# Performance work log

Measured on AMD Instinct MI355X. Metric: run time of the kernel, lower is better.

The kernel has to match this reference:

```python
import jax, jax.numpy as jnp
import numpy as np

B, S, NH = 8, 32, 8
N = S * S + 1            # 1 extra (cls) token + S*S image tokens
C = 512
D = C // NH
SCALE = D ** -0.5
LAM = 0.6


def _ln(x, w, b, eps=1e-5):
    m = x.mean(-1, keepdims=True)
    v = ((x - m) ** 2).mean(-1, keepdims=True)
    return (x - m) / jnp.sqrt(v + eps) * w + b


def _rel_index():
    ch, cw = np.meshgrid(np.arange(S), np.arange(S), indexing='ij')
    cf = np.stack([ch.ravel(), cw.ravel()])            # [2, S*S]
    rel = (cf[:, :, None] - cf[:, None, :]).transpose(1, 2, 0).astype(np.int64)
    rel[..., 0] += S - 1
    rel[..., 1] += S - 1
    rel[..., 0] *= 2 * S - 1
    idx = rel.sum(-1)                                  # [n, n]
    out = np.zeros((N, N), dtype=np.int64)             # F.pad with 0 for extra token row/col
    out[1:, 1:] = idx
    return jnp.asarray(out)


def setup_inputs():
    key = jax.random.key(0)
    ks = jax.random.split(key, 8)
    std = 0.02
    return {
        'x': jax.random.normal(ks[0], (B, N, C), jnp.float32),
        'ln1_w': jnp.ones((C,), jnp.float32), 'ln1_b': jnp.zeros((C,), jnp.float32),
        'qkv_w': jax.random.normal(ks[1], (3 * C, C), jnp.float32) * std,
        'rpb_table': jax.random.normal(ks[2], ((2 * S - 1) * (2 * S - 1) + 1, NH), jnp.float32) * std,
        'proj_w': jax.random.normal(ks[3], (C, C), jnp.float32) * std,
        'proj_b': jnp.zeros((C,), jnp.float32),
        'token_weights': jnp.array([0.5, 0.5], jnp.float32),
        'ln2_w': jnp.ones((C,), jnp.float32), 'ln2_b': jnp.zeros((C,), jnp.float32),
        'fc1_w': jax.random.normal(ks[4], (4 * C, C), jnp.float32) * std,
        'fc1_b': jnp.zeros((4 * C,), jnp.float32),
        'fc2_w': jax.random.normal(ks[5], (C, 4 * C), jnp.float32) * std,
        'fc2_b': jnp.zeros((C,), jnp.float32),
        'rel_index': _rel_index(),
        'H': S, 'W': S,
    }


def _attn_core(xn, qkv_w, rpb_table, rel_index):
    qkv = (xn @ qkv_w.T).reshape(B, N, 3, NH, D).transpose(2, 0, 3, 1, 4)
    q, k, v = qkv[0] * SCALE, qkv[1], qkv[2]           # [B, NH, N, D]
    bias = rpb_table[rel_index].transpose(2, 0, 1)     # [NH, N, N] bias-table gather
    attn = jax.nn.softmax(jnp.einsum('bhnd,bhmd->bhnm', q, k) + bias[None], axis=-1)
    out = jnp.einsum('bhnm,bhmd->bhnd', attn, v).transpose(0, 2, 1, 3).reshape(B, N, C)
    return attn, out


def _plan(attn, token_weights):
    # Non-differentiable token-selection plan (pure index computation).
    a = np.asarray(attn)
    cls = a[:, :, 0, 1:].mean(axis=1)                  # [B, n] head-averaged cls->image attn
    n = cls.shape[1]
    avg = cls.mean(1, keepdims=True)
    mx = cls.max(1, keepdims=True)
    counts = ((cls >= avg) & (cls <= mx)).sum(1)
    max_value = int(counts.max())
    T = float(counts.mean())
    sig = 1.0 / (1.0 + np.exp(-(max_value - T) / B))
    keep = int(round(n * (LAM + (1.0 - LAM) * sig)))
    top = np.argsort(-cls, axis=1)[:, :keep].reshape(-1)   # per-batch top-k, flattened
    _, first = np.unique(top, return_index=True)
    sel = top[np.sort(first)][:keep]                   # dedup (first occurrence), truncate
    remaining = N - (1 + keep)
    w = np.asarray(jax.nn.softmax(token_weights))
    nt = int(w[0] * remaining)
    ni = remaining - nt
    kk = jax.random.key(1234)
    ti = jax.random.randint(kk, (B, nt), 0, 1)         # text pool has exactly 1 token
    ii = jax.random.randint(jax.random.fold_in(kk, 1), (B, ni), 0, n - 1)
    return jnp.asarray(sel), ti, ii


def _gather_tok(t, idx):
    return jnp.take_along_axis(t, jnp.broadcast_to(idx[:, :, None], idx.shape + (t.shape[-1],)), axis=1)


def _assemble(xo, xn, sel, ti, ii):
    parts = [xo[:, :1], xo[:, 1:][:, sel],             # kept extra + selected image tokens
             _gather_tok(xn[:, 1:2], ti),              # random 'text' filler from y=xn
             _gather_tok(xn[:, 2:], ii)]               # random 'image' filler from y=xn
    return jnp.concatenate(parts, axis=1)


def reference(x, ln1_w, ln1_b, qkv_w, rpb_table, proj_w, proj_b, token_weights, ln2_w, ln2_b, fc1_w, fc1_b, fc2_w, fc2_b, rel_index, H, W):
    xn = _ln(x, ln1_w, ln1_b)
    attn, out = _attn_core(xn, qkv_w, rpb_table, rel_index)
    xo = out @ proj_w.T + proj_b
    sel, ti, ii = _plan(attn, token_weights)
    x1 = x + _assemble(xo, xn, sel, ti, ii)
    h = _ln(x1, ln2_w, ln2_b)
    h = jax.nn.gelu(h @ fc1_w.T + fc1_b, approximate=False)
    return x1 + (h @ fc2_w.T + fc2_b)
```

## Files before the change

### kernel.cpp

```cpp
#include <hip/hip_runtime.h>
#include <cmath>

#define PARTITIONABLE 1

constexpr int B_ = 8;
constexpr int N_ = 1025;
constexpr int C_ = 512;
constexpr int NH_ = 8;
constexpr int D_ = 64;
constexpr int K3_ = 1536;
constexpr int F_ = 2048;
constexpr int ROWS_ = B_ * N_;
constexpr int NXCD_ = 8;
constexpr int WCONV_BLKS_ = (K3_ * C_ + C_ * C_ + F_ * C_ + C_ * F_) / 1024;

constexpr size_t BYTE_XN      = 0;
constexpr size_t BYTE_QKVBF   = 16793600;
constexpr size_t BYTE_XNBF    = 41984000;
constexpr size_t BYTE_HBUF    = 16793600;
constexpr size_t BYTE_WTAIL   = 60882944;
constexpr size_t BYTE_ATTNBF  = 67174400;
constexpr size_t BYTE_X1NBF   = 75571200;
constexpr size_t BYTE_XO      = 83968000;
constexpr size_t BYTE_X1      = 100761600;
constexpr size_t PLAN_BYTE    = 117555200;

typedef unsigned short u16;
typedef __attribute__((ext_vector_type(4))) unsigned short u16x4;
typedef __attribute__((ext_vector_type(8))) short bf16x8;
typedef __attribute__((ext_vector_type(4))) float f32x4;

__device__ inline u16 f2bf(float f) {
  unsigned u = __float_as_uint(f);
  u = (u + 0x7FFFu + ((u >> 16) & 1u)) >> 16;
  return (u16)u;
}
__device__ inline float bf2f(u16 u) { return __uint_as_float(((unsigned)u) << 16); }

__device__ inline int xcd_swz(int bid, int nwg) {
  const int xcd = bid % NXCD_, i = bid / NXCD_;
  const int q = nwg / NXCD_, r = nwg % NXCD_;
  const int base = (xcd < r) ? xcd * (q + 1) : r * (q + 1) + (xcd - r) * q;
  return base + i;
}

__device__ inline void gload_lds16(const void* g, void* l) {
  __builtin_amdgcn_global_load_lds(
      (const __attribute__((address_space(1))) void*)g,
      (__attribute__((address_space(3))) void*)l, 16, 0, 0);
}

__global__ __launch_bounds__(256) void ln_wconv_kernel(
    const float* __restrict__ x, const float* __restrict__ w,
    const float* __restrict__ b, float* __restrict__ of, u16* __restrict__ ob,
    const float* __restrict__ w0, const float* __restrict__ w1,
    const float* __restrict__ w2, const float* __restrict__ w3,
    u16* __restrict__ o0, u16* __restrict__ o1,
    u16* __restrict__ o2, u16* __restrict__ o3) {
  __shared__ float red[4];
  if (blockIdx.x >= ROWS_) {
    constexpr int n0 = K3_ * C_, n1 = C_ * C_, n2 = F_ * C_;
    const int idx4 = ((blockIdx.x - ROWS_) * 256 + threadIdx.x) * 4;
    const float* src;
    u16* dst;
    int off;
    if (idx4 < n0) { src = w0; dst = o0; off = idx4; }
    else if (idx4 < n0 + n1) { src = w1; dst = o1; off = idx4 - n0; }
    else if (idx4 < n0 + n1 + n2) { src = w2; dst = o2; off = idx4 - n0 - n1; }
    else { src = w3; dst = o3; off = idx4 - n0 - n1 - n2; }
    const float4 v = *(const float4*)(src + off);
    u16x4 r;
    r.x = f2bf(v.x); r.y = f2bf(v.y); r.z = f2bf(v.z); r.w = f2bf(v.w);
    *(u16x4*)(dst + off) = r;
    return;
  }
  const int r = blockIdx.x;
  const int t = threadIdx.x;
  const float* xr = x + (size_t)r * C_;
  float v0 = xr[t], v1 = xr[t + 256];
  float s = v0 + v1;
#pragma unroll
  for (int o = 32; o; o >>= 1) s += __shfl_down(s, o);
  if ((t & 63) == 0) red[t >> 6] = s;
  __syncthreads();
  const float mean = (red[0] + red[1] + red[2] + red[3]) * (1.0f / 512.0f);
  __syncthreads();
  const float d0 = v0 - mean, d1 = v1 - mean;
  float q = d0 * d0 + d1 * d1;
#pragma unroll
  for (int o = 32; o; o >>= 1) q += __shfl_down(q, o);
  if ((t & 63) == 0) red[t >> 6] = q;
  __syncthreads();
  const float var = (red[0] + red[1] + red[2] + red[3]) * (1.0f / 512.0f);
  const float inv = 1.0f / sqrtf(var + 1e-5f);
  const float r0 = d0 * inv * w[t] + b[t];
  const float r1 = d1 * inv * w[t + 256] + b[t + 256];
  of[(size_t)r * C_ + t] = r0;
  of[(size_t)r * C_ + t + 256] = r1;
  ob[(size_t)r * C_ + t] = f2bf(r0);
  ob[(size_t)r * C_ + t + 256] = f2bf(r1);
}

template <int BN, int ACT, bool RES, bool OUTBF, bool QSCALE, bool PLANQ0>
__global__ __launch_bounds__(256) void gemm_bf_kernel(
    const u16* __restrict__ A, const u16* __restrict__ W,
    const float* __restrict__ bias, const float* __restrict__ resid,
    void* __restrict__ outp, int M, int K, int Nout, int ngemm,
    const float* __restrict__ xnf, const float* __restrict__ qkvwf,
    double* __restrict__ q0o) {
  constexpr int WN = BN / 2;
  constexpr int NJ = WN / 16;
  constexpr int BPW = (BN / 8) / 4;
  __shared__ alignas(16) u16 As[2][128][64];
  __shared__ alignas(16) u16 Bs[2][BN][64];
  if (PLANQ0 && (int)blockIdx.x >= ngemm) {
    const int idx = ((int)blockIdx.x - ngemm) * 256 + threadIdx.x;
    const int b = idx >> 9, hd = idx & 511;
    const float* xr = xnf + (size_t)(b * N_) * C_;
    const float* wr = qkvwf + (size_t)hd * C_;
    double s = 0.0;
    for (int c = 0; c < C_; c += 4) {
      const float4 xv = *(const float4*)(xr + c);
      const float4 wv = *(const float4*)(wr + c);
      s += (double)xv.x * (double)wv.x;
      s += (double)xv.y * (double)wv.y;
      s += (double)xv.z * (double)wv.z;
      s += (double)xv.w * (double)wv.w;
    }
    q0o[idx] = s * 0.125;
    return;
  }
  const int tid = threadIdx.x;
  const int ny = Nout / BN;
  const int l = xcd_swz(blockIdx.x, ngemm);
  const int m0 = (l / ny) * 128, n0 = (l % ny) * BN;
  const int wave = tid >> 6, lane = tid & 63;
  const int wr = wave >> 1, wc = wave & 1;
  const int lrow = lane & 15, lgrp = lane >> 4;
  const int srow = lane >> 3;
  const int soff = (16 * (lane & 7)) ^ (16 * srow);
  const int nk = K >> 6;

  auto stage = [&](int k0, int bufi) {
#pragma unroll
    for (int c = 0; c < 4; ++c) {
      const int q = wave * 4 + c;
      const int row = q * 8 + srow;
      int gm = m0 + row;
      if (gm >= M) gm = M - 1;
      gload_lds16((const char*)(A + (size_t)gm * K + k0) + soff,
                  (char*)&As[bufi][0][0] + (q << 10));
    }
#pragma unroll
    for (int c = 0; c < BPW; ++c) {
      const int q = wave * BPW + c;
      const int row = q * 8 + srow;
      gload_lds16((const char*)(W + (size_t)(n0 + row) * K + k0) + soff,
                  (char*)&Bs[bufi][0][0] + (q << 10));
    }
  };

  f32x4 acc[4][NJ] = {};
  stage(0, 0);
  int buf = 0;
  for (int t = 0; t < nk; ++t) {
    if (t + 1 < nk) {
      stage((t + 1) << 6, buf ^ 1);
      if constexpr (BN == 128) asm volatile("s_waitcnt vmcnt(8)" ::: "memory");
      else                     asm volatile("s_waitcnt vmcnt(6)" ::: "memory");
    } else {
      asm volatile("s_waitcnt vmcnt(0)" ::: "memory");
    }
    __builtin_amdgcn_sched_barrier(0);
    __builtin_amdgcn_s_barrier();
    const char* asb = (const char*)&As[buf][0][0];
    const char* bsb = (const char*)&Bs[buf][0][0];
    __builtin_amdgcn_s_setprio(1);
#pragma unroll
    for (int ch = 0; ch < 2; ++ch) {
      bf16x8 af[4], bfv[NJ];
#pragma unroll
      for (int i = 0; i < 4; ++i) {
        const int ra = wr * 64 + i * 16 + lrow;
        const int cb = ch * 64 + lgrp * 16;
        af[i] = *(const bf16x8*)(asb + (ra << 7) + (cb ^ ((ra & 7) << 4)));
      }
#pragma unroll
      for (int j = 0; j < NJ; ++j) {
        const int rb = wc * WN + j * 16 + lrow;
        const int cb = ch * 64 + lgrp * 16;
        bfv[j] = *(const bf16x8*)(bsb + (rb << 7) + (cb ^ ((rb & 7) << 4)));
      }
#pragma unroll
      for (int i = 0; i < 4; ++i)
#pragma unroll
        for (int j = 0; j < NJ; ++j)
          acc[i][j] = __builtin_amdgcn_mfma_f32_16x16x32_bf16(af[i], bfv[j], acc[i][j], 0, 0, 0);
    }
    __builtin_amdgcn_s_setprio(0);
    asm volatile("s_waitcnt lgkmcnt(0)" ::: "memory");
    __builtin_amdgcn_sched_barrier(0);
    __builtin_amdgcn_s_barrier();
    buf ^= 1;
  }
#pragma unroll
  for (int i = 0; i < 4; ++i) {
#pragma unroll
    for (int j = 0; j < NJ; ++j) {
#pragma unroll
      for (int reg = 0; reg < 4; ++reg) {
        const int gm = m0 + wr * 64 + i * 16 + lgrp * 4 + reg;
        if (gm >= M) continue;
        const int gn = n0 + wc * WN + j * 16 + lrow;
        float v = acc[i][j][reg];
        if (bias) v += bias[gn];
        if (ACT == 1) v = 0.5f * v * (1.0f + erff(v * 0.70710678118654752440f));
        if (QSCALE) { if (gn < 512) v *= 0.125f; }
        if (RES) v += resid[(size_t)gm * Nout + gn];
        if (OUTBF) ((u16*)outp)[(size_t)gm * Nout + gn] = f2bf(v);
        else       ((float*)outp)[(size_t)gm * Nout + gn] = v;
      }
    }
  }
}

__global__ __launch_bounds__(256) void pack_kv_kernel(const u16* __restrict__ qkvbf,
                                                      u16* __restrict__ kb,
                                                      u16* __restrict__ vb,
                                                      const float* __restrict__ qkvwf,
                                                      const double* __restrict__ q0,
                                                      double* __restrict__ u,
                                                      int npack) {
  if ((int)blockIdx.x >= npack) {
    const int idx = ((int)blockIdx.x - npack) * 256 + threadIdx.x;
    const int b = idx >> 12, h = (idx >> 9) & 7, c = idx & 511;
    double s = 0.0;
    for (int d = 0; d < D_; ++d)
      s += q0[b * 512 + h * 64 + d] * (double)qkvwf[(size_t)(512 + h * 64 + d) * C_ + c];
    u[idx] = s;
    return;
  }
  const int tile = blockIdx.x & 15, h = (blockIdx.x >> 4) & 7, b = (int)blockIdx.x >> 7;
  const int t = threadIdx.x;
  __shared__ u16 Vt[64][72];
  const int krow = tile * 64 + (t >> 2);
  const int dseg = (t & 3) * 16;
  const u16* p = qkvbf + (size_t)(b * N_ + krow) * K3_ + 512 + h * D_ + dseg;
  const bf16x8 k0 = *(const bf16x8*)p;
  const bf16x8 k1 = *(const bf16x8*)(p + 8);
  u16* kp = kb + ((size_t)(b * NH_ + h) * 1024 + krow) * 64 + dseg;
  *(bf16x8*)kp = k0;
  *(bf16x8*)(kp + 8) = k1;
  const bf16x8 v0 = *(const bf16x8*)(p + 512);
  const bf16x8 v1 = *(const bf16x8*)(p + 520);
  *(bf16x8*)(&Vt[t >> 2][dseg]) = v0;
  *(bf16x8*)(&Vt[t >> 2][dseg + 8]) = v1;
  __syncthreads();
  const int d = t >> 2, kseg = (t & 3) * 16;
  bf16x8 o0, o1;
#pragma unroll
  for (int i = 0; i < 8; ++i) o0[i] = (short)Vt[kseg + i][d];
#pragma unroll
  for (int i = 0; i < 8; ++i) o1[i] = (short)Vt[kseg + 8 + i][d];
  u16* vp = vb + ((size_t)(b * NH_ + h) * 64 + d) * 1024 + tile * 64 + kseg;
  *(bf16x8*)vp = o0;
  *(bf16x8*)(vp + 8) = o1;
}

__global__ __launch_bounds__(384) void attn_mfma_kernel(
    const u16* __restrict__ qkvbf, const u16* __restrict__ kb,
    const u16* __restrict__ vb, const float* __restrict__ rpb,
    u16* __restrict__ attnout) {
  const int l = xcd_swz(blockIdx.x, gridDim.x);
  const int qt = l % 11;
  const int bh = l / 11;
  const int h = bh & 7, b = bh >> 3;
  const int wave = threadIdx.x >> 6, lane = threadIdx.x & 63;
  const int lrow = lane & 15, lgrp = lane >> 4;
  const int qblk = qt * 96;
  const int qbase = qblk + wave * 16;
  __shared__ alignas(16) u16 Ks[2][64][64];
  __shared__ alignas(16) u16 Vs[2][64][64];
  __shared__ alignas(16) u16 Pl[6][16][74];
  __shared__ u16 tab[36 * 63];

  const u16* kpan = kb + (size_t)(b * NH_ + h) * 1024 * 64;
  const u16* vpan = vb + (size_t)(b * NH_ + h) * 64 * 1024;

  if (wave < 4) {
#pragma unroll
    for (int c = 0; c < 2; ++c) {
      const int q = wave * 2 + c;
      const int Y = (q << 10) | (lane << 4);
      const int Ys = Y ^ (((Y >> 7) & 7) << 4);
      gload_lds16((const char*)kpan + Ys, (char*)&Ks[0][0][0] + (q << 10));
    }
  } else {
#pragma unroll
    for (int c = 0; c < 4; ++c) {
      const int q = (wave - 4) * 4 + c;
      const int Y = (q << 10) | (lane << 4);
      const int Ys = Y ^ (((Y >> 7) & 7) << 4);
      const int row = Y >> 7;
      gload_lds16((const char*)vpan + (size_t)row * 2048 + (Ys & 127),
                  (char*)&Vs[0][0][0] + (q << 10));
    }
  }

  const int qimin = max(qblk - 1, 0);
  const int qimax = min(qblk + 94, 1023);
  const int qymin = qimin >> 5;
  const int qymax = qimax >> 5;
  const int nrows = qymax - qymin + 32;
  for (int i = threadIdx.x; i < nrows * 63; i += 384)
    tab[i] = f2bf(rpb[(size_t)(qymin * 63 + i) * NH_ + h]);

  u16 (*pl)[74] = Pl[wave];

  bf16x8 qf[2];
  {
    const int qrow = min(qbase + lrow, N_ - 1);
    const u16* qp = qkvbf + (size_t)(b * N_ + qrow) * K3_ + h * D_;
    qf[0] = *(const bf16x8*)(qp + lgrp * 8);
    qf[1] = *(const bf16x8*)(qp + 32 + lgrp * 8);
  }

  const float bias0 = rpb[h];

  int AlocR[4];
  bool qclsR[4];
#pragma unroll
  for (int reg = 0; reg < 4; ++reg) {
    const int qr = min(qbase + lgrp * 4 + reg, N_ - 1);
    const int qi = max(qr - 1, 0);
    AlocR[reg] = ((qi >> 5) - qymin + 31) * 63 + (qi & 31) + 31;
    qclsR[reg] = (qr == 0);
  }

  f32x4 psum = {0.f, 0.f, 0.f, 0.f};
  f32x4 o[4] = {};

  __syncthreads();

  for (int t = 0; t < 16; ++t) {
    const int buf = t & 1;
    if (t < 15) {
      const int keybase2 = (t + 1) * 64;
      if (wave < 4) {
#pragma unroll
        for (int c = 0; c < 2; ++c) {
          const int q = wave * 2 + c;
          const int Y = (q << 10) | (lane << 4);
          const int Ys = Y ^ (((Y >> 7) & 7) << 4);
          gload_lds16((const char*)kpan + ((size_t)keybase2 << 7) + Ys,
                      (char*)&Ks[buf ^ 1][0][0] + (q << 10));
        }
        asm volatile("s_waitcnt vmcnt(2)" ::: "memory");
      } else {
#pragma unroll
        for (int c = 0; c < 4; ++c) {
          const int q = (wave - 4) * 4 + c;
          const int Y = (q << 10) | (lane << 4);
          const int Ys = Y ^ (((Y >> 7) & 7) << 4);
          const int row = Y >> 7;
          gload_lds16((const char*)vpan + (size_t)row * 2048 + ((size_t)keybase2 << 1) + (Ys & 127),
                      (char*)&Vs[buf ^ 1][0][0] + (q << 10));
        }
        asm volatile("s_waitcnt vmcnt(4)" ::: "memory");
      }
    } else {
      asm volatile("s_waitcnt vmcnt(0)" ::: "memory");
    }
    __builtin_amdgcn_sched_barrier(0);
    __builtin_amdgcn_s_barrier();

    const int keybase = t * 64;
    const char* ksb = (const char*)&Ks[buf][0][0];
    const char* vsb = (const char*)&Vs[buf][0][0];

    f32x4 s[4] = {};
    __builtin_amdgcn_s_setprio(1);
#pragma unroll
    for (int tile = 0; tile < 4; ++tile) {
      const int row = tile * 16 + lrow;
      const int sw = (row & 7) << 4;
      const bf16x8 kf0 = *(const bf16x8*)(ksb + ((row * 128 + lgrp * 16) ^ sw));
      const bf16x8 kf1 = *(const bf16x8*)(ksb + ((row * 128 + 64 + lgrp * 16) ^ sw));
      s[tile] = __builtin_amdgcn_mfma_f32_16x16x32_bf16(qf[0], kf0, s[tile], 0, 0, 0);
      s[tile] = __builtin_amdgcn_mfma_f32_16x16x32_bf16(qf[1], kf1, s[tile], 0, 0, 0);
    }
    __builtin_amdgcn_s_setprio(0);
#pragma unroll
    for (int tile = 0; tile < 4; ++tile) {
      const int key = keybase + tile * 16 + lrow;
      const int ki = max(key - 1, 0);
      const int kpart = (ki >> 5) * 63 + (ki & 31);
      const bool kcls = (key == 0);
#pragma unroll
      for (int reg = 0; reg < 4; ++reg) {
        const float bias = (qclsR[reg] || kcls) ? bias0 : bf2f(tab[AlocR[reg] - kpart]);
        const float p = __expf(s[tile][reg] + bias);
        psum[reg] += p;
        pl[lgrp * 4 + reg][tile * 16 + lrow] = f2bf(p);
      }
    }
    __builtin_amdgcn_s_setprio(1);
#pragma unroll
    for (int ch = 0; ch < 2; ++ch) {
      const bf16x8 pf = *(const bf16x8*)(&pl[lrow][ch * 32 + lgrp * 8]);
#pragma unroll
      for (int dt = 0; dt < 4; ++dt) {
        const int row = dt * 16 + lrow;
        const bf16x8 vf = *(const bf16x8*)(vsb + ((row * 128 + ch * 64 + lgrp * 16) ^ ((row & 7) << 4)));
        o[dt] = __builtin_amdgcn_mfma_f32_16x16x32_bf16(pf, vf, o[dt], 0, 0, 0);
      }
    }
    __builtin_amdgcn_s_setprio(0);
    asm volatile("s_waitcnt lgkmcnt(0)" ::: "memory");
    __builtin_amdgcn_sched_barrier(0);
    __builtin_amdgcn_s_barrier();
  }

#pragma unroll
  for (int reg = 0; reg < 4; ++reg) {
    float v = psum[reg];
    v += __shfl_xor(v, 1);
    v += __shfl_xor(v, 2);
    v += __shfl_xor(v, 4);
    v += __shfl_xor(v, 8);
    psum[reg] = v;
  }

  float ptail;
  {
    const u16* k1p = qkvbf + (size_t)(b * N_ + 1024) * K3_ + 512 + h * D_;
    const bf16x8 k10 = *(const bf16x8*)(k1p + lgrp * 8);
    const bf16x8 k11 = *(const bf16x8*)(k1p + 32 + lgrp * 8);
    float part = 0.f;
#pragma unroll
    for (int i = 0; i < 8; ++i)
      part += bf2f((u16)qf[0][i]) * bf2f((u16)k10[i]) + bf2f((u16)qf[1][i]) * bf2f((u16)k11[i]);
    part += __shfl_xor(part, 16);
    part += __shfl_xor(part, 32);
    const int q_s = min(qbase + lrow, N_ - 1);
    const int qi_s = max(q_s - 1, 0);
    const int Aloc_s = ((qi_s >> 5) - qymin + 31) * 63 + (qi_s & 31) + 31;
    const float btail = (q_s == 0) ? bias0 : bf2f(tab[Aloc_s - 31 * 63 - 31]);
    ptail = __expf(part + btail);
  }

  float v1024[4];
#pragma unroll
  for (int dt = 0; dt < 4; ++dt)
    v1024[dt] = bf2f(qkvbf[(size_t)(b * N_ + 1024) * K3_ + 1024 + h * D_ + dt * 16 + lrow]);

#pragma unroll
  for (int reg = 0; reg < 4; ++reg) {
    const float pr = __shfl(ptail, lgrp * 4 + reg);
    const int qrow = qbase + lgrp * 4 + reg;
    if (qrow >= N_) continue;
    const float inv = 1.0f / (psum[reg] + pr);
    u16* op = attnout + (size_t)(b * N_ + qrow) * C_ + h * D_ + lrow;
#pragma unroll
    for (int dt = 0; dt < 4; ++dt)
      op[dt * 16] = f2bf((o[dt][reg] + pr * v1024[dt]) * inv);
  }
}

__global__ __launch_bounds__(128) void plan_logit_kernel(const float* __restrict__ xn,
                                                         const double* __restrict__ u,
                                                         double* __restrict__ lgt) {
  __shared__ double ul[8][512];
  const int b = blockIdx.y;
  const int m = blockIdx.x * 128 + threadIdx.x;
  for (int i = threadIdx.x; i < 4096; i += 128)
    ((double*)ul)[i] = u[(size_t)b * 4096 + i];
  __syncthreads();
  if (m >= N_) return;
  const float* xr = xn + (size_t)(b * N_ + m) * C_;
  double s[8] = {};
  for (int c = 0; c < C_; c += 4) {
    const float4 xv = *(const float4*)(xr + c);
#pragma unroll
    for (int hh = 0; hh < 8; ++hh) {
      s[hh] += (double)xv.x * ul[hh][c];
      s[hh] += (double)xv.y * ul[hh][c + 1];
      s[hh] += (double)xv.z * ul[hh][c + 2];
      s[hh] += (double)xv.w * ul[hh][c + 3];
    }
  }
#pragma unroll
  for (int hh = 0; hh < 8; ++hh)
    lgt[(size_t)(b * 8 + hh) * N_ + m] = s[hh];
}

__global__ __launch_bounds__(256) void plan_softmax_kernel(const double* __restrict__ lgt,
                                                           double* __restrict__ mxz) {
  __shared__ double red[4];
  const int bh = blockIdx.x, t = threadIdx.x;
  const double* row = lgt + (size_t)bh * N_;
  double m = -1e300;
  for (int i = t; i < N_; i += 256) m = fmax(m, row[i]);
#pragma unroll
  for (int o = 32; o; o >>= 1) m = fmax(m, __shfl_down(m, o));
  if ((t & 63) == 0) red[t >> 6] = m;
  __syncthreads();
  const double mx = fmax(fmax(red[0], red[1]), fmax(red[2], red[3]));
  __syncthreads();
  double z = 0.0;
  for (int i = t; i < N_; i += 256) z += exp(row[i] - mx);
#pragma unroll
  for (int o = 32; o; o >>= 1) z += __shfl_down(z, o);
  if ((t & 63) == 0) red[t >> 6] = z;
  __syncthreads();
  if (t == 0) {
    mxz[bh] = mx;
    mxz[64 + bh] = red[0] + red[1] + red[2] + red[3];
  }
}

__global__ __launch_bounds__(256) void plan_cls_kernel(const double* __restrict__ lgt,
                                                       const double* __restrict__ mxz,
                                                       double* __restrict__ cls) {
  const int idx = blockIdx.x * 256 + threadIdx.x;
  const int b = idx >> 10, i = idx & 1023;
  double s = 0.0;
  for (int h = 0; h < 8; ++h) {
    const int bh = b * 8 + h;
    s += exp(lgt[(size_t)bh * N_ + 1 + i] - mxz[bh]) / mxz[64 + bh];
  }
  cls[idx] = s / 8.0;
}

__device__ inline void tf2x32(unsigned k0, unsigned k1, unsigned& x0, unsigned& x1) {
  const unsigned ks2 = k0 ^ k1 ^ 0x1BD11BDAu;
  const int r0[4] = {13, 15, 26, 6};
  const int r1[4] = {17, 29, 16, 24};
  x0 += k0; x1 += k1;
#pragma unroll
  for (int i = 0; i < 4; ++i) { x0 += x1; x1 = (x1 << r0[i]) | (x1 >> (32 - r0[i])); x1 ^= x0; }
  x0 += k1; x1 += ks2 + 1u;
#pragma unroll
  for (int i = 0; i < 4; ++i) { x0 += x1; x1 = (x1 << r1[i]) | (x1 >> (32 - r1[i])); x1 ^= x0; }
  x0 += ks2; x1 += k0 + 2u;
#pragma unroll
  for (int i = 0; i < 4; ++i) { x0 += x1; x1 = (x1 << r0[i]) | (x1 >> (32 - r0[i])); x1 ^= x0; }
  x0 += k0; x1 += k1 + 3u;
#pragma unroll
  for (int i = 0; i < 4; ++i) { x0 += x1; x1 = (x1 << r1[i]) | (x1 >> (32 - r1[i])); x1 ^= x0; }
  x0 += k1; x1 += ks2 + 4u;
#pragma unroll
  for (int i = 0; i < 4; ++i) { x0 += x1; x1 = (x1 << r0[i]) | (x1 >> (32 - r0[i])); x1 ^= x0; }
  x0 += ks2; x1 += k0 + 5u;
}

__global__ __launch_bounds__(1024) void plan_tail_kernel(
    const double* __restrict__ cls, const float* __restrict__ tw,
    int* __restrict__ scal, int* __restrict__ sel, int* __restrict__ ii) {
  __shared__ double sv[1024];
  __shared__ int sid[1024];
  __shared__ double dred8[8][16];
  __shared__ double mred8[8][16];
  __shared__ int ired8[8][16];
  __shared__ double stats2[8][2];
  __shared__ int sc3[3];
  const int t = threadIdx.x;
  const int wid = t >> 6, lane = t & 63;

  double v = cls[t];
  int idx = t;
  for (int k = 2; k <= 1024; k <<= 1) {
    for (int j = k >> 1; j > 0; j >>= 1) {
      const bool desc = ((t & k) == 0);
      const bool iAmLow = (t & j) == 0;
      double ov;
      int oi;
      if (j >= 64) {
        sv[t] = v;
        sid[t] = idx;
        __syncthreads();
        ov = sv[t ^ j];
        oi = sid[t ^ j];
        __syncthreads();
      } else {
        ov = __shfl_xor(v, j);
        oi = __shfl_xor(idx, j);
      }
      const bool myFirst = (v > ov) || (v == ov && idx < oi);
      const bool keepMine = desc ? (iAmLow == myFirst) : (iAmLow != myFirst);
      if (!keepMine) { v = ov; idx = oi; }
    }
  }
  sel[t] = idx;

  double val8[8];
#pragma unroll
  for (int b = 0; b < 8; ++b) val8[b] = cls[b * 1024 + t];
#pragma unroll
  for (int b = 0; b < 8; ++b) {
    double s = val8[b];
#pragma unroll
    for (int o = 32; o; o >>= 1) s += __shfl_down(s, o);
    if (lane == 0) dred8[b][wid] = s;
    double mv = val8[b];
#pragma unroll
    for (int o = 32; o; o >>= 1) mv = fmax(mv, __shfl_down(mv, o));
    if (lane == 0) mred8[b][wid] = mv;
  }
  __syncthreads();
  if (t < 8) {
    double tot = 0;
    for (int i = 0; i < 16; ++i) tot += dred8[t][i];
    stats2[t][0] = tot / 1024.0;
    double mx = mred8[t][0];
    for (int i = 1; i < 16; ++i) mx = fmax(mx, mred8[t][i]);
    stats2[t][1] = mx;
  }
  __syncthreads();
#pragma unroll
  for (int b = 0; b < 8; ++b) {
    int c = (val8[b] >= stats2[b][0] && val8[b] <= stats2[b][1]) ? 1 : 0;
#pragma unroll
    for (int o = 32; o; o >>= 1) c += __shfl_down(c, o);
    if (lane == 0) ired8[b][wid] = c;
  }
  __syncthreads();

  if (t == 0) {
    int maxv = 0;
    double sum = 0.0;
    for (int b = 0; b < 8; ++b) {
      int cc = 0;
      for (int i = 0; i < 16; ++i) cc += ired8[b][i];
      maxv = max(maxv, cc);
      sum += (double)cc;
    }
    const double T = sum / 8.0;
    const double sig = 1.0 / (1.0 + exp(-((double)maxv - T) / 8.0));
    const double keepf = 1024.0 * (0.6 + (1.0 - 0.6) * sig);
    const int keep = __double2int_rn(keepf);
    const int remaining = 1024 - keep;
    const float t0 = tw[0], t1 = tw[1];
    const float mw = fmaxf(t0, t1);
    const float e0 = expf(t0 - mw), e1 = expf(t1 - mw);
    const float w0 = e0 / (e0 + e1);
    const int nt = (int)(w0 * (float)remaining);
    const int ni = remaining - nt;
    scal[0] = keep; scal[1] = nt; scal[2] = ni;
    sc3[0] = keep; sc3[1] = nt; sc3[2] = ni;
  }
  __syncthreads();

  const int ni = sc3[2];
  const int size = 8 * ni;
  const unsigned span = 1023u;
  unsigned mult = 65536u % span;
  mult = (mult * mult) % span;
  unsigned f0 = 0u, f1 = 1u;
  tf2x32(0u, 1234u, f0, f1);
#if PARTITIONABLE
  unsigned k1a = 0u, k1b = 0u;
  tf2x32(f0, f1, k1a, k1b);
  unsigned k2a = 0u, k2b = 1u;
  tf2x32(f0, f1, k2a, k2b);
  for (int i = t; i < size; i += 1024) {
    unsigned h0 = 0u, h1 = (unsigned)i;
    tf2x32(k1a, k1b, h0, h1);
    const unsigned hb = h0 ^ h1;
    unsigned l0 = 0u, l1 = (unsigned)i;
    tf2x32(k2a, k2b, l0, l1);
    const unsigned lb = l0 ^ l1;
    ii[i] = (int)(((hb % span) * mult + (lb % span)) % span);
  }
#else
  unsigned a0 = 0u, a1 = 2u;
  tf2x32(f0, f1, a0, a1);
  unsigned b0 = 1u, b1 = 3u;
  tf2x32(f0, f1, b0, b1);
  const int half = size >> 1;
  for (int i = t; i < half; i += 1024) {
    unsigned h0 = (unsigned)i, h1 = (unsigned)(i + half);
    tf2x32(a0, b0, h0, h1);
    unsigned l0 = (unsigned)i, l1 = (unsigned)(i + half);
    tf2x32(a1, b1, l0, l1);
    ii[i]        = (int)(((h0 % span) * mult + (l0 % span)) % span);
    ii[i + half] = (int)(((h1 % span) * mult + (l1 % span)) % span);
  }
#endif
}

__global__ __launch_bounds__(256) void assemble_ln_kernel(
    const float* __restrict__ x, const float* __restrict__ xn,
    const float* __restrict__ xo, const int* __restrict__ scal,
    const int* __restrict__ sel, const int* __restrict__ ii,
    const float* __restrict__ w, const float* __restrict__ bb,
    float* __restrict__ x1, u16* __restrict__ ob) {
  __shared__ float red[4];
  const int blk = blockIdx.x;
  const int b = blk / N_, tok = blk % N_;
  const int keep = scal[0], nt = scal[1], ni = scal[2];
  const float* src;
  if (tok == 0) {
    src = xo + (size_t)(b * N_) * C_;
  } else if (tok <= keep) {
    src = xo + (size_t)(b * N_ + 1 + sel[tok - 1]) * C_;
  } else if (tok <= keep + nt) {
    src = xn + (size_t)(b * N_ + 1) * C_;
  } else {
    const int j = tok - 1 - keep - nt;
    src = xn + (size_t)(b * N_ + 2 + ii[b * ni + j]) * C_;
  }
  const int t = threadIdx.x;
  const size_t o = (size_t)blk * C_;
  const float v0 = x[o + t] + src[t];
  const float v1 = x[o + t + 256] + src[t + 256];
  x1[o + t] = v0;
  x1[o + t + 256] = v1;
  float s = v0 + v1;
#pragma unroll
  for (int of = 32; of; of >>= 1) s += __shfl_down(s, of);
  if ((t & 63) == 0) red[t >> 6] = s;
  __syncthreads();
  const float mean = (red[0] + red[1] + red[2] + red[3]) * (1.0f / 512.0f);
  __syncthreads();
  const float d0 = v0 - mean, d1 = v1 - mean;
  float q = d0 * d0 + d1 * d1;
#pragma unroll
  for (int of = 32; of; of >>= 1) q += __shfl_down(q, of);
  if ((t & 63) == 0) red[t >> 6] = q;
  __syncthreads();
  const float var = (red[0] + red[1] + red[2] + red[3]) * (1.0f / 512.0f);
  const float inv = 1.0f / sqrtf(var + 1e-5f);
  ob[o + t] = f2bf(d0 * inv * w[t] + bb[t]);
  ob[o + t + 256] = f2bf(d1 * inv * w[t + 256] + bb[t + 256]);
}

extern "C" void kernel_launch(void* const* d_in, const int* in_sizes, int n_in,
                              void* d_out, int out_size, void* d_ws, size_t ws_size,
                              hipStream_t stream) {
  (void)in_sizes; (void)n_in; (void)out_size; (void)ws_size;
  const float* x     = (const float*)d_in[0];
  const float* ln1w  = (const float*)d_in[1];
  const float* ln1b  = (const float*)d_in[2];
  const float* qkvw  = (const float*)d_in[3];
  const float* rpb   = (const float*)d_in[4];
  const float* projw = (const float*)d_in[5];
  const float* projb = (const float*)d_in[6];
  const float* tw    = (const float*)d_in[7];
  const float* ln2w  = (const float*)d_in[8];
  const float* ln2b  = (const float*)d_in[9];
  const float* fc1w  = (const float*)d_in[10];
  const float* fc1b  = (const float*)d_in[11];
  const float* fc2w  = (const float*)d_in[12];
  const float* fc2b  = (const float*)d_in[13];
  float* out = (float*)d_out;
  char* base = (char*)d_ws;

  float* xn       = (float*)(base + BYTE_XN);
  u16*   qkv_bf   = (u16*)(base + BYTE_QKVBF);
  u16*   xn_bf    = (u16*)(base + BYTE_XNBF);
  u16*   hbuf     = (u16*)(base + BYTE_HBUF);
  u16*   wq_bf    = (u16*)(base + BYTE_WTAIL);
  u16*   wp_bf    = wq_bf + K3_ * C_;
  u16*   w1_bf    = wp_bf + C_ * C_;
  u16*   w2_bf    = w1_bf + F_ * C_;
  u16*   attn_bf  = (u16*)(base + BYTE_ATTNBF);
  u16*   x1n_bf   = (u16*)(base + BYTE_X1NBF);
  float* xo       = (float*)(base + BYTE_XO);
  u16*   kbuf     = (u16*)(base + BYTE_X1);
  u16*   vbuf     = kbuf + (size_t)B_ * NH_ * 1024 * 64;
  float* x1       = (float*)(base + BYTE_X1);

  char* pb = base + PLAN_BYTE;
  double* q0  = (double*)pb;
  double* u   = q0 + 4096;
  double* lgt = u + 32768;
  double* mxz = lgt + 65600;
  double* cls = mxz + 128;
  int* counts = (int*)(cls + 8192);
  int* scal   = counts + 8;
  int* sel    = scal + 4;
  int* iibuf  = sel + 1024;

  ln_wconv_kernel<<<ROWS_ + WCONV_BLKS_, 256, 0, stream>>>(
      x, ln1w, ln1b, xn, xn_bf,
      qkvw, projw, fc1w, fc2w, wq_bf, wp_bf, w1_bf, w2_bf);
  gemm_bf_kernel<128, 0, false, true, true, true><<<65 * 12 + 16, 256, 0, stream>>>(
      xn_bf, wq_bf, nullptr, nullptr, qkv_bf, ROWS_, C_, K3_, 65 * 12,
      xn, qkvw, q0);
  pack_kv_kernel<<<1024 + 128, 256, 0, stream>>>(
      qkv_bf, kbuf, vbuf, qkvw, q0, u, 1024);
  plan_logit_kernel<<<dim3(9, B_), 128, 0, stream>>>(xn, u, lgt);
  plan_softmax_kernel<<<64, 256, 0, stream>>>(lgt, mxz);
  plan_cls_kernel<<<32, 256, 0, stream>>>(lgt, mxz, cls);
  plan_tail_kernel<<<1, 1024, 0, stream>>>(cls, tw, scal, sel, iibuf);
  attn_mfma_kernel<<<11 * NH_ * B_, 384, 0, stream>>>(
      qkv_bf, kbuf, vbuf, rpb, attn_bf);
  gemm_bf_kernel<64, 0, false, false, false, false><<<65 * 8, 256, 0, stream>>>(
      attn_bf, wp_bf, projb, nullptr, xo, ROWS_, C_, C_, 65 * 8,
      nullptr, nullptr, nullptr);
  assemble_ln_kernel<<<ROWS_, 256, 0, stream>>>(
      x, xn, xo, scal, sel, iibuf, ln2w, ln2b, x1, x1n_bf);
  gemm_bf_kernel<128, 1, false, true, false, false><<<65 * 16, 256, 0, stream>>>(
      x1n_bf, w1_bf, fc1b, nullptr, hbuf, ROWS_, C_, F_, 65 * 16,
      nullptr, nullptr, nullptr);
  gemm_bf_kernel<64, 0, true, false, false, false><<<65 * 8, 256, 0, stream>>>(
      hbuf, w2_bf, fc2b, x1, out, ROWS_, F_, C_, 65 * 8,
      nullptr, nullptr, nullptr);
}
```

Measured before the change: 346.2 us.

## Fold plan logit and softmax kernels into attention and proj GEMM launches

The plan-logit computation now runs as 24 extra blocks appended to the attention kernel launch, and the plan row softmax runs as 64 extra blocks appended to the projection GEMM launch. This removes two separate kernel launches and lets the small plan work overlap with the big kernels. The logit blocks no longer stage u in shared memory and read it straight from global, and they use 384-thread blocks. The cost is some extra per-block divergence in the large kernels.

```diff
diff --git a/kernel.cpp b/kernel.cpp
--- a/kernel.cpp
+++ b/kernel.cpp
@@ -101,13 +101,14 @@
   ob[(size_t)r * C_ + t + 256] = f2bf(r1);
 }
 
-template <int BN, int ACT, bool RES, bool OUTBF, bool QSCALE, bool PLANQ0>
+template <int BN, int ACT, bool RES, bool OUTBF, bool QSCALE, bool PLANQ0, bool SMAX>
 __global__ __launch_bounds__(256) void gemm_bf_kernel(
     const u16* __restrict__ A, const u16* __restrict__ W,
     const float* __restrict__ bias, const float* __restrict__ resid,
     void* __restrict__ outp, int M, int K, int Nout, int ngemm,
     const float* __restrict__ xnf, const float* __restrict__ qkvwf,
-    double* __restrict__ q0o) {
+    double* __restrict__ q0o,
+    const double* __restrict__ lgtp, double* __restrict__ mxzp) {
   constexpr int WN = BN / 2;
   constexpr int NJ = WN / 16;
   constexpr int BPW = (BN / 8) / 4;
@@ -130,6 +131,31 @@
     q0o[idx] = s * 0.125;
     return;
   }
+  if (SMAX && (int)blockIdx.x >= ngemm) {
+    __shared__ double red[4];
+    const int bh = (int)blockIdx.x - ngemm;
+    const int t = threadIdx.x;
+    const double* row = lgtp + (size_t)bh * N_;
+    double m = -1e300;
+    for (int i = t; i < N_; i += 256) m = fmax(m, row[i]);
+#pragma unroll
+    for (int o = 32; o; o >>= 1) m = fmax(m, __shfl_down(m, o));
+    if ((t & 63) == 0) red[t >> 6] = m;
+    __syncthreads();
+    const double mx = fmax(fmax(red[0], red[1]), fmax(red[2], red[3]));
+    __syncthreads();
+    double z = 0.0;
+    for (int i = t; i < N_; i += 256) z += exp(row[i] - mx);
+#pragma unroll
+    for (int o = 32; o; o >>= 1) z += __shfl_down(z, o);
+    if ((t & 63) == 0) red[t >> 6] = z;
+    __syncthreads();
+    if (t == 0) {
+      mxzp[bh] = mx;
+      mxzp[64 + bh] = red[0] + red[1] + red[2] + red[3];
+    }
+    return;
+  }
   const int tid = threadIdx.x;
   const int ny = Nout / BN;
   const int l = xcd_swz(blockIdx.x, ngemm);
@@ -270,8 +296,37 @@
 __global__ __launch_bounds__(384) void attn_mfma_kernel(
     const u16* __restrict__ qkvbf, const u16* __restrict__ kb,
     const u16* __restrict__ vb, const float* __restrict__ rpb,
-    u16* __restrict__ attnout) {
-  const int l = xcd_swz(blockIdx.x, gridDim.x);
+    u16* __restrict__ attnout,
+    const float* __restrict__ xnf, const double* __restrict__ uu,
+    double* __restrict__ lgt, int nattn) {
+  __shared__ alignas(16) u16 Ks[2][64][64];
+  __shared__ alignas(16) u16 Vs[2][64][64];
+  __shared__ alignas(16) u16 Pl[6][16][74];
+  __shared__ u16 tab[36 * 63];
+  if ((int)blockIdx.x >= nattn) {
+    const int lb = (int)blockIdx.x - nattn;
+    const int b = lb / 3, part = lb % 3;
+    const int m = part * 384 + threadIdx.x;
+    if (m >= N_) return;
+    const float* xr = xnf + (size_t)(b * N_ + m) * C_;
+    const double* ub = uu + (size_t)b * 4096;
+    double s[8] = {};
+    for (int c = 0; c < C_; c += 4) {
+      const float4 xv = *(const float4*)(xr + c);
+#pragma unroll
+      for (int hh = 0; hh < 8; ++hh) {
+        s[hh] += (double)xv.x * ub[hh * 512 + c];
+        s[hh] += (double)xv.y * ub[hh * 512 + c + 1];
+        s[hh] += (double)xv.z * ub[hh * 512 + c + 2];
+        s[hh] += (double)xv.w * ub[hh * 512 + c + 3];
+      }
+    }
+#pragma unroll
+    for (int hh = 0; hh < 8; ++hh)
+      lgt[(size_t)(b * 8 + hh) * N_ + m] = s[hh];
+    return;
+  }
+  const int l = xcd_swz(blockIdx.x, nattn);
   const int qt = l % 11;
   const int bh = l / 11;
   const int h = bh & 7, b = bh >> 3;
@@ -279,10 +334,6 @@
   const int lrow = lane & 15, lgrp = lane >> 4;
   const int qblk = qt * 96;
   const int qbase = qblk + wave * 16;
-  __shared__ alignas(16) u16 Ks[2][64][64];
-  __shared__ alignas(16) u16 Vs[2][64][64];
-  __shared__ alignas(16) u16 Pl[6][16][74];
-  __shared__ u16 tab[36 * 63];
 
   const u16* kpan = kb + (size_t)(b * NH_ + h) * 1024 * 64;
   const u16* vpan = vb + (size_t)(b * NH_ + h) * 64 * 1024;
@@ -464,58 +515,6 @@
 #pragma unroll
     for (int dt = 0; dt < 4; ++dt)
       op[dt * 16] = f2bf((o[dt][reg] + pr * v1024[dt]) * inv);
-  }
-}
-
-__global__ __launch_bounds__(128) void plan_logit_kernel(const float* __restrict__ xn,
-                                                         const double* __restrict__ u,
-                                                         double* __restrict__ lgt) {
-  __shared__ double ul[8][512];
-  const int b = blockIdx.y;
-  const int m = blockIdx.x * 128 + threadIdx.x;
-  for (int i = threadIdx.x; i < 4096; i += 128)
-    ((double*)ul)[i] = u[(size_t)b * 4096 + i];
-  __syncthreads();
-  if (m >= N_) return;
-  const float* xr = xn + (size_t)(b * N_ + m) * C_;
-  double s[8] = {};
-  for (int c = 0; c < C_; c += 4) {
-    const float4 xv = *(const float4*)(xr + c);
-#pragma unroll
-    for (int hh = 0; hh < 8; ++hh) {
-      s[hh] += (double)xv.x * ul[hh][c];
-      s[hh] += (double)xv.y * ul[hh][c + 1];
-      s[hh] += (double)xv.z * ul[hh][c + 2];
-      s[hh] += (double)xv.w * ul[hh][c + 3];
-    }
-  }
-#pragma unroll
-  for (int hh = 0; hh < 8; ++hh)
-    lgt[(size_t)(b * 8 + hh) * N_ + m] = s[hh];
-}
-
-__global__ __launch_bounds__(256) void plan_softmax_kernel(const double* __restrict__ lgt,
-                                                           double* __restrict__ mxz) {
-  __shared__ double red[4];
-  const int bh = blockIdx.x, t = threadIdx.x;
-  const double* row = lgt + (size_t)bh * N_;
-  double m = -1e300;
-  for (int i = t; i < N_; i += 256) m = fmax(m, row[i]);
-#pragma unroll
-  for (int o = 32; o; o >>= 1) m = fmax(m, __shfl_down(m, o));
-  if ((t & 63) == 0) red[t >> 6] = m;
-  __syncthreads();
-  const double mx = fmax(fmax(red[0], red[1]), fmax(red[2], red[3]));
-  __syncthreads();
-  double z = 0.0;
-  for (int i = t; i < N_; i += 256) z += exp(row[i] - mx);
-#pragma unroll
-  for (int o = 32; o; o >>= 1) z += __shfl_down(z, o);
-  if ((t & 63) == 0) red[t >> 6] = z;
-  __syncthreads();
-  if (t == 0) {
-    mxz[bh] = mx;
-    mxz[64 + bh] = red[0] + red[1] + red[2] + red[3];
   }
 }
 
@@ -785,26 +784,24 @@
   ln_wconv_kernel<<<ROWS_ + WCONV_BLKS_, 256, 0, stream>>>(
       x, ln1w, ln1b, xn, xn_bf,
       qkvw, projw, fc1w, fc2w, wq_bf, wp_bf, w1_bf, w2_bf);
-  gemm_bf_kernel<128, 0, false, true, true, true><<<65 * 12 + 16, 256, 0, stream>>>(
+  gemm_bf_kernel<128, 0, false, true, true, true, false><<<65 * 12 + 16, 256, 0, stream>>>(
       xn_bf, wq_bf, nullptr, nullptr, qkv_bf, ROWS_, C_, K3_, 65 * 12,
-      xn, qkvw, q0);
+      xn, qkvw, q0, nullptr, nullptr);
   pack_kv_kernel<<<1024 + 128, 256, 0, stream>>>(
       qkv_bf, kbuf, vbuf, qkvw, q0, u, 1024);
-  plan_logit_kernel<<<dim3(9, B_), 128, 0, stream>>>(xn, u, lgt);
-  plan_softmax_kernel<<<64, 256, 0, stream>>>(lgt, mxz);
+  attn_mfma_kernel<<<11 * NH_ * B_ + 24, 384, 0, stream>>>(
+      qkv_bf, kbuf, vbuf, rpb, attn_bf, xn, u, lgt, 11 * NH_ * B_);
+  gemm_bf_kernel<64, 0, false, false, false, false, true><<<65 * 8 + 64, 256, 0, stream>>>(
+      attn_bf, wp_bf, projb, nullptr, xo, ROWS_, C_, C_, 65 * 8,
+      nullptr, nullptr, nullptr, lgt, mxz);
   plan_cls_kernel<<<32, 256, 0, stream>>>(lgt, mxz, cls);
   plan_tail_kernel<<<1, 1024, 0, stream>>>(cls, tw, scal, sel, iibuf);
-  attn_mfma_kernel<<<11 * NH_ * B_, 384, 0, stream>>>(
-      qkv_bf, kbuf, vbuf, rpb, attn_bf);
-  gemm_bf_kernel<64, 0, false, false, false, false><<<65 * 8, 256, 0, stream>>>(
-      attn_bf, wp_bf, projb, nullptr, xo, ROWS_, C_, C_, 65 * 8,
-      nullptr, nullptr, nullptr);
   assemble_ln_kernel<<<ROWS_, 256, 0, stream>>>(
       x, xn, xo, scal, sel, iibuf, ln2w, ln2b, x1, x1n_bf);
-  gemm_bf_kernel<128, 1, false, true, false, false><<<65 * 16, 256, 0, stream>>>(
+  gemm_bf_kernel<128, 1, false, true, false, false, false><<<65 * 16, 256, 0, stream>>>(
       x1n_bf, w1_bf, fc1b, nullptr, hbuf, ROWS_, C_, F_, 65 * 16,
-      nullptr, nullptr, nullptr);
-  gemm_bf_kernel<64, 0, true, false, false, false><<<65 * 8, 256, 0, stream>>>(
+      nullptr, nullptr, nullptr, nullptr, nullptr);
+  gemm_bf_kernel<64, 0, true, false, false, false, false><<<65 * 8, 256, 0, stream>>>(
       hbuf, w2_bf, fc2b, x1, out, ROWS_, F_, C_, 65 * 8,
-      nullptr, nullptr, nullptr);
-}
+      nullptr, nullptr, nullptr, nullptr, nullptr);
+}
```

After: 341.3 us. No clear change (-1.4%).
